# Kernel tuning notes

Measured on AMD Instinct MI355X. Metric: run time of the kernel, lower is better.

## Reference

```python
import jax, jax.numpy as jnp
import numpy as np
from jax import lax

H, E = 32, 10
ZS, ZC = 8, 8
XS, XC = 5, 2
AS, AC = 1, 4
T, N = 256, 2048


def setup_inputs() -> dict:
    key = jax.random.key(0)
    ks = jax.random.split(key, 16)
    s = 0.1
    inp = {
        'x': jax.random.uniform(ks[0], (T, N, XS, XC), jnp.float32),
        'a': jax.random.uniform(ks[1], (T, N, AS, AC), jnp.float32),
        'h0': jax.random.normal(ks[2], (N, H), jnp.float32),
        # gumbel noise for categorical sampling (argmax trick)
        'gumbel': -jnp.log(-jnp.log(jax.random.uniform(ks[3], (T, N, ZS, ZC), jnp.float32, 1e-6, 1.0 - 1e-6))),
        # Encoder: Linear(H+E -> ZS*ZC)
        'enc_W': jax.random.normal(ks[4], (ZS * ZC, H + E), jnp.float32) * s,
        'enc_b': jnp.zeros((ZS * ZC,), jnp.float32),
        # GRUCell(input = ZS*ZC + AS*AC, hidden = H)
        'gru_Wih': jax.random.normal(ks[5], (3 * H, ZS * ZC + AS * AC), jnp.float32) * s,
        'gru_Whh': jax.random.normal(ks[6], (3 * H, H), jnp.float32) * s,
        'gru_bih': jnp.zeros((3 * H,), jnp.float32),
        'gru_bhh': jnp.zeros((3 * H,), jnp.float32),
        # Decoder: Linear(H + ZS*ZC -> XS*XC)
        'dec_W': jax.random.normal(ks[7], (XS * XC, H + ZS * ZC), jnp.float32) * s,
        'dec_b': jnp.zeros((XS * XC,), jnp.float32),
        # DynamicsPredictor: Linear(H -> ZS*ZC)
        'dyn_W': jax.random.normal(ks[8], (ZS * ZC, H), jnp.float32) * s,
        'dyn_b': jnp.zeros((ZS * ZC,), jnp.float32),
        # RewardPredictor: Linear(H -> 1, no bias)
        'rew_W': jax.random.normal(ks[9], (1, H), jnp.float32) * s,
        # ContinuePredictor: Linear(H -> 1)
        'con_W': jax.random.normal(ks[10], (1, H), jnp.float32) * s,
        'con_b': jnp.zeros((1,), jnp.float32),
    }
    return inp


def _gru(x_in, h, Wih, Whh, bih, bhh):
    gi = x_in @ Wih.T + bih  # [N, 3H]
    gh = h @ Whh.T + bhh
    i_r, i_z, i_n = jnp.split(gi, 3, axis=-1)
    h_r, h_z, h_n = jnp.split(gh, 3, axis=-1)
    r = jax.nn.sigmoid(i_r + h_r)
    z = jax.nn.sigmoid(i_z + h_z)
    n = jnp.tanh(i_n + r * h_n)
    return (1.0 - z) * n + z * h


def _st_sample(logits, g):
    # OneHotCategorical straight-through sample via gumbel-argmax
    idx = jnp.argmax(logits + g, axis=-1)
    onehot = jax.nn.one_hot(idx, ZC, dtype=logits.dtype)
    probs = jax.nn.softmax(logits, axis=-1)
    return probs + lax.stop_gradient(onehot - probs)


def reference(x, a, h0, gumbel, enc_W, enc_b, gru_Wih, gru_Whh, gru_bih, gru_bhh,
              dec_W, dec_b, dyn_W, dyn_b, rew_W, con_W, con_b):
    e = x.reshape(T, N, XS * XC)        # embedder = flatten(-2)
    a_flat = a.reshape(T, N, AS * AC)

    def enc(h, e_t):
        return (jnp.concatenate([h, e_t], axis=-1) @ enc_W.T + enc_b).reshape(-1, ZS, ZC)

    zl0 = enc(h0, e[0])
    z0 = _st_sample(zl0, gumbel[0])

    def step(carry, inp):
        h_prev, z_prev = carry
        e_t, a_prev, g_t = inp
        za = jnp.concatenate([z_prev.reshape(N, ZS * ZC), a_prev], axis=-1)
        h_t = _gru(za, h_prev, gru_Wih, gru_Whh, gru_bih, gru_bhh)
        zl_t = enc(h_t, e_t)
        z_t = _st_sample(zl_t, g_t)
        return (h_t, z_t), (h_t, zl_t, z_t)

    _, (hs, zls, zs) = lax.scan(step, (h0, z0), (e[1:], a_flat[:-1], gumbel[1:]))
    h = jnp.concatenate([h0[None], hs], axis=0)                  # [T,N,H]
    z_prior_logits = jnp.concatenate([zl0[None], zls], axis=0)   # [T,N,ZS,ZC]
    z = jnp.concatenate([z0[None], zs], axis=0)                  # [T,N,ZS,ZC]

    hz = jnp.concatenate([h, z.reshape(T, N, ZS * ZC)], axis=-1)
    x_logits = (hz @ dec_W.T + dec_b).reshape(T, N, XS, XC)
    z_post_logits = (h @ dyn_W.T + dyn_b).reshape(T, N, ZS, ZC)
    r_loc = h @ rew_W.T                 # Normal loc, scale=1
    c_logits = h @ con_W.T + con_b      # Bernoulli logits
    return (x_logits, r_loc, c_logits, z_prior_logits, z_post_logits)
```

## Files before the change

kernel.cpp:

```cpp
#include <hip/hip_runtime.h>


#define TT 256
#define NB 2048
#define HH 32
#define ZD 64
#define XDm 10
#define ADm 4
#define GIN 68
#define EIN 42

#define SWHH_S 36
#define SWIH_S 97
#define SENC_S 44
#define SDYN_S 36
#define SDEC_S 100
#define SH_S   36
#define SZ_S   68

#define OFF_X   0ul
#define OFF_R   5242880ul
#define OFF_C   5767168ul
#define OFF_ZPL 6291456ul
#define OFF_ZPO 39845888ul

__device__ __forceinline__ float sigmoid_f(float v) { return 1.f / (1.f + __expf(-v)); }
__device__ __forceinline__ void nt_store(float* p, float v) { __builtin_nontemporal_store(v, p); }

extern "C" __global__ void __launch_bounds__(256)
rssm_fused(const float* __restrict__ x, const float* __restrict__ a,
           const float* __restrict__ h0, const float* __restrict__ gum,
           const float* __restrict__ encW, const float* __restrict__ encB,
           const float* __restrict__ Wih, const float* __restrict__ Whh,
           const float* __restrict__ bih, const float* __restrict__ bhh,
           const float* __restrict__ decW, const float* __restrict__ decB,
           const float* __restrict__ dynW, const float* __restrict__ dynB,
           const float* __restrict__ rewW, const float* __restrict__ conW,
           const float* __restrict__ conB, float* __restrict__ out)
{
    __shared__ __align__(16) float sWhh[96 * SWHH_S];
    __shared__ float sWih[GIN * SWIH_S];
    __shared__ __align__(16) float sEnc[64 * SENC_S];
    __shared__ __align__(16) float sDyn[64 * SDYN_S];
    __shared__ __align__(16) float sDec[10 * SDEC_S];
    __shared__ float sBih[96], sBhh[96], sEncB[64], sDynB[64], sDecB[16];
    __shared__ float sRew[32], sCon[32], sConB;
    __shared__ __align__(16) float sH[8 * SH_S];
    __shared__ float sVal[8 * 9];
    __shared__ int   sIdx[8 * 9];
    __shared__ float sZL[8 * SZ_S];
    __shared__ float sZP[8 * SZ_S];

    const int tid = threadIdx.x;

    for (int i = tid; i < 96 * HH; i += 256) { int j = i >> 5, k = i & 31; sWhh[j * SWHH_S + k] = Whh[i]; }
    for (int i = tid; i < 96 * GIN; i += 256) { int j = i / GIN, c = i - j * GIN; sWih[c * SWIH_S + j] = Wih[i]; }
    for (int i = tid; i < 64 * EIN; i += 256) { int j = i / EIN, c = i - j * EIN; sEnc[j * SENC_S + c] = encW[i]; }
    for (int i = tid; i < 64 * HH; i += 256) { int j = i >> 5, k = i & 31; sDyn[j * SDYN_S + k] = dynW[i]; }
    for (int i = tid; i < 10 * 96; i += 256) { int j = i / 96, c = i - j * 96; sDec[j * SDEC_S + c] = decW[i]; }
    if (tid < 96) { sBih[tid] = bih[tid]; sBhh[tid] = bhh[tid]; }
    if (tid >= 96 && tid < 160) { sEncB[tid - 96] = encB[tid - 96]; sDynB[tid - 96] = dynB[tid - 96]; }
    if (tid >= 160 && tid < 170) sDecB[tid - 160] = decB[tid - 160];
    if (tid >= 192 && tid < 224) sRew[tid - 192] = rewW[tid - 192];
    if (tid >= 224) sCon[tid - 224] = conW[tid - 224];
    if (tid == 170) sConB = conB[0];

    const int e    = tid & 7;
    const int slot = tid >> 3;
    const int w    = slot >> 3;
    const int r    = slot & 7;
    const int n0   = blockIdx.x * 8;
    const int n    = n0 + e;

    { int ee = tid >> 5, k = tid & 31; sH[ee * SH_S + k] = h0[(n0 + ee) * HH + k]; }
    __syncthreads();

    float h[HH];
#pragma unroll
    for (int k = 0; k < HH; k += 4) {
        float4 v = *(const float4*)&sH[e * SH_S + k];
        h[k] = v.x; h[k + 1] = v.y; h[k + 2] = v.z; h[k + 3] = v.w;
    }
    float h_own = sH[e * SH_S + slot];

    const float* xptr = x   + (size_t)n * XDm;
    const float* gptr = gum + (size_t)n * ZD;
    const float* aptr = a   + (size_t)n * ADm;

    float et[XDm], ap[ADm];
    float g1, g2;
#pragma unroll
    for (int m = 0; m < XDm; ++m) et[m] = xptr[m];
    g1 = gptr[8 * w + r];
    g2 = gptr[32 + 8 * w + r];
#pragma unroll
    for (int m = 0; m < ADm; ++m) ap[m] = 0.f;

#pragma unroll 1
    for (int t = 0; t < TT; ++t) {
        float etn[XDm], apn[ADm], g1n = 0.f, g2n = 0.f;
        if (t + 1 < TT) {
            const float* xp = xptr + (size_t)(t + 1) * (NB * XDm);
#pragma unroll
            for (int m = 0; m < XDm; ++m) etn[m] = xp[m];
            const float* gp = gptr + (size_t)(t + 1) * (NB * ZD);
            g1n = gp[8 * w + r];
            g2n = gp[32 + 8 * w + r];
            const float* app = aptr + (size_t)t * (NB * ADm);
#pragma unroll
            for (int m = 0; m < ADm; ++m) apn[m] = app[m];
        } else {
#pragma unroll
            for (int m = 0; m < XDm; ++m) etn[m] = 0.f;
#pragma unroll
            for (int m = 0; m < ADm; ++m) apn[m] = 0.f;
        }

        if (t > 0) {
            float vhr = 0.f, vhz = 0.f, vhn = 0.f;
            const float4* wr = (const float4*)&sWhh[slot * SWHH_S];
            const float4* wz = (const float4*)&sWhh[(32 + slot) * SWHH_S];
            const float4* wn = (const float4*)&sWhh[(64 + slot) * SWHH_S];
#pragma unroll
            for (int kk = 0; kk < 8; ++kk) {
                float4 wa = wr[kk], wb = wz[kk], wc = wn[kk];
                vhr = fmaf(wa.x, h[4 * kk], vhr); vhr = fmaf(wa.y, h[4 * kk + 1], vhr);
                vhr = fmaf(wa.z, h[4 * kk + 2], vhr); vhr = fmaf(wa.w, h[4 * kk + 3], vhr);
                vhz = fmaf(wb.x, h[4 * kk], vhz); vhz = fmaf(wb.y, h[4 * kk + 1], vhz);
                vhz = fmaf(wb.z, h[4 * kk + 2], vhz); vhz = fmaf(wb.w, h[4 * kk + 3], vhz);
                vhn = fmaf(wc.x, h[4 * kk], vhn); vhn = fmaf(wc.y, h[4 * kk + 1], vhn);
                vhn = fmaf(wc.z, h[4 * kk + 2], vhn); vhn = fmaf(wc.w, h[4 * kk + 3], vhn);
            }
            float vir = 0.f, viz = 0.f, vin = 0.f;
#pragma unroll
            for (int s = 0; s < 8; ++s) {
                int   c = 8 * s + sIdx[e * 9 + s];
                float v = sVal[e * 9 + s];
                const float* wc = &sWih[c * SWIH_S];
                vir = fmaf(wc[slot], v, vir);
                viz = fmaf(wc[32 + slot], v, viz);
                vin = fmaf(wc[64 + slot], v, vin);
            }
#pragma unroll
            for (int m = 0; m < ADm; ++m) {
                const float* wc = &sWih[(64 + m) * SWIH_S];
                float av = ap[m];
                vir = fmaf(wc[slot], av, vir);
                viz = fmaf(wc[32 + slot], av, viz);
                vin = fmaf(wc[64 + slot], av, vin);
            }
            float gir = vir + sBih[slot],      ghr = vhr + sBhh[slot];
            float giz = viz + sBih[32 + slot], ghz = vhz + sBhh[32 + slot];
            float gnn = vin + sBih[64 + slot], ghn = vhn + sBhh[64 + slot];
            float rg = sigmoid_f(gir + ghr);
            float zg = sigmoid_f(giz + ghz);
            float ng = tanhf(gnn + rg * ghn);
            float hn_ = (1.f - zg) * ng + zg * h_own;
            sH[e * SH_S + slot] = hn_;
        }
        __syncthreads();
        if (t > 0) {
#pragma unroll
            for (int k = 0; k < HH; k += 4) {
                float4 v = *(const float4*)&sH[e * SH_S + k];
                h[k] = v.x; h[k + 1] = v.y; h[k + 2] = v.z; h[k + 3] = v.w;
            }
            h_own = sH[e * SH_S + slot];
        }

        float z1 = 0.f, z2 = 0.f;
        {
            const float4* e1 = (const float4*)&sEnc[slot * SENC_S];
            const float4* e2 = (const float4*)&sEnc[(32 + slot) * SENC_S];
#pragma unroll
            for (int kk = 0; kk < 8; ++kk) {
                float4 wa = e1[kk], wb = e2[kk];
                z1 = fmaf(wa.x, h[4 * kk], z1); z1 = fmaf(wa.y, h[4 * kk + 1], z1);
                z1 = fmaf(wa.z, h[4 * kk + 2], z1); z1 = fmaf(wa.w, h[4 * kk + 3], z1);
                z2 = fmaf(wb.x, h[4 * kk], z2); z2 = fmaf(wb.y, h[4 * kk + 1], z2);
                z2 = fmaf(wb.z, h[4 * kk + 2], z2); z2 = fmaf(wb.w, h[4 * kk + 3], z2);
            }
            const float* e1s = &sEnc[slot * SENC_S + 32];
            const float* e2s = &sEnc[(32 + slot) * SENC_S + 32];
#pragma unroll
            for (int m = 0; m < XDm; ++m) {
                z1 = fmaf(e1s[m], et[m], z1);
                z2 = fmaf(e2s[m], et[m], z2);
            }
            z1 += sEncB[slot];
            z2 += sEncB[32 + slot];
        }

        float mx1 = z1, mx2 = z2;
#pragma unroll
        for (int d = 8; d < 64; d <<= 1) {
            mx1 = fmaxf(mx1, __shfl_xor(mx1, d));
            mx2 = fmaxf(mx2, __shfl_xor(mx2, d));
        }
        float key1 = z1 + g1; int ki1 = r;
        float key2 = z2 + g2; int ki2 = r;
#pragma unroll
        for (int d = 8; d < 64; d <<= 1) {
            float ok = __shfl_xor(key1, d); int oi = __shfl_xor(ki1, d);
            if (ok > key1 || (ok == key1 && oi < ki1)) { key1 = ok; ki1 = oi; }
            float ok2 = __shfl_xor(key2, d); int oi2 = __shfl_xor(ki2, d);
            if (ok2 > key2 || (ok2 == key2 && oi2 < ki2)) { key2 = ok2; ki2 = oi2; }
        }
        float p1 = __expf(z1 - mx1), p2 = __expf(z2 - mx2);
        float s1 = p1, s2 = p2;
#pragma unroll
        for (int d = 8; d < 64; d <<= 1) {
            s1 += __shfl_xor(s1, d);
            s2 += __shfl_xor(s2, d);
        }
        float pk1 = __shfl(p1, e + 8 * ki1) / s1;
        float pk2 = __shfl(p2, e + 8 * ki2) / s2;
        if (r == 0) {
            sVal[e * 9 + w]     = pk1 + (1.f - pk1); sIdx[e * 9 + w]     = ki1;
            sVal[e * 9 + 4 + w] = pk2 + (1.f - pk2); sIdx[e * 9 + 4 + w] = ki2;
        }
        sZL[e * SZ_S + slot]      = z1;
        sZL[e * SZ_S + 32 + slot] = z2;

        {
            float d1 = 0.f, d2 = 0.f;
            const float4* q1 = (const float4*)&sDyn[slot * SDYN_S];
            const float4* q2 = (const float4*)&sDyn[(32 + slot) * SDYN_S];
#pragma unroll
            for (int kk = 0; kk < 8; ++kk) {
                float4 wa = q1[kk], wb = q2[kk];
                d1 = fmaf(wa.x, h[4 * kk], d1); d1 = fmaf(wa.y, h[4 * kk + 1], d1);
                d1 = fmaf(wa.z, h[4 * kk + 2], d1); d1 = fmaf(wa.w, h[4 * kk + 3], d1);
                d2 = fmaf(wb.x, h[4 * kk], d2); d2 = fmaf(wb.y, h[4 * kk + 1], d2);
                d2 = fmaf(wb.z, h[4 * kk + 2], d2); d2 = fmaf(wb.w, h[4 * kk + 3], d2);
            }
            sZP[e * SZ_S + slot]      = d1 + sDynB[slot];
            sZP[e * SZ_S + 32 + slot] = d2 + sDynB[32 + slot];
        }

        __syncthreads();

        if (slot < 10) {
            const float* dw = &sDec[slot * SDEC_S];
            float acc = 0.f;
#pragma unroll
            for (int k = 0; k < HH; ++k) acc = fmaf(dw[k], h[k], acc);
#pragma unroll
            for (int s = 0; s < 8; ++s)
                acc = fmaf(dw[32 + 8 * s + sIdx[e * 9 + s]], sVal[e * 9 + s], acc);
            acc += sDecB[slot];
            nt_store(&out[OFF_X + ((size_t)t * NB + n) * XDm + slot], acc);
        } else if (slot == 10) {
            float acc = 0.f;
#pragma unroll
            for (int k = 0; k < HH; ++k) acc = fmaf(sRew[k], h[k], acc);
            nt_store(&out[OFF_R + (size_t)t * NB + n], acc);
        } else if (slot == 11) {
            float acc = 0.f;
#pragma unroll
            for (int k = 0; k < HH; ++k) acc = fmaf(sCon[k], h[k], acc);
            nt_store(&out[OFF_C + (size_t)t * NB + n], acc + sConB);
        }

        {
            size_t rowbase = (size_t)t * NB + n0;
            int f1 = tid, f2 = tid + 256;
            int ee1 = f1 >> 6, c1 = f1 & 63, ee2 = f2 >> 6, c2 = f2 & 63;
            nt_store(&out[OFF_ZPL + (rowbase + ee1) * ZD + c1], sZL[ee1 * SZ_S + c1]);
            nt_store(&out[OFF_ZPL + (rowbase + ee2) * ZD + c2], sZL[ee2 * SZ_S + c2]);
            nt_store(&out[OFF_ZPO + (rowbase + ee1) * ZD + c1], sZP[ee1 * SZ_S + c1]);
            nt_store(&out[OFF_ZPO + (rowbase + ee2) * ZD + c2], sZP[ee2 * SZ_S + c2]);
        }

#pragma unroll
        for (int m = 0; m < XDm; ++m) et[m] = etn[m];
#pragma unroll
        for (int m = 0; m < ADm; ++m) ap[m] = apn[m];
        g1 = g1n; g2 = g2n;
    }
}

extern "C" void kernel_launch(void* const* d_in, const int* in_sizes, int n_in,
                              void* d_out, int out_size, void* d_ws, size_t ws_size,
                              hipStream_t stream) {
    const float* x    = (const float*)d_in[0];
    const float* a    = (const float*)d_in[1];
    const float* h0   = (const float*)d_in[2];
    const float* gumb = (const float*)d_in[3];
    const float* encW = (const float*)d_in[4];
    const float* encB = (const float*)d_in[5];
    const float* Wih  = (const float*)d_in[6];
    const float* Whh  = (const float*)d_in[7];
    const float* bih  = (const float*)d_in[8];
    const float* bhh  = (const float*)d_in[9];
    const float* decW = (const float*)d_in[10];
    const float* decB = (const float*)d_in[11];
    const float* dynW = (const float*)d_in[12];
    const float* dynB = (const float*)d_in[13];
    const float* rewW = (const float*)d_in[14];
    const float* conW = (const float*)d_in[15];
    const float* conB = (const float*)d_in[16];

    rssm_fused<<<NB / 8, 256, 0, stream>>>(x, a, h0, gumb, encW, encB, Wih, Whh,
                                           bih, bhh, decW, decB, dynW, dynB,
                                           rewW, conW, conB, (float*)d_out);
}
```

Baseline: 1.191 ms.

## Map one batch element per wavefront to remove block-wide barriers

Restructures the recurrent kernel so that each 64-lane wavefront owns one batch element, where before 8 elements were spread across the whole 256-thread block. The per-step block barriers and the shared buffers for logits and samples are replaced by wave shuffles and register copies. Each lane now computes one encoder and one dynamics output, and the output stores are issued directly and coalesced. The grid doubles and the launch bounds request two blocks per CU. The cost is that each lane runs longer serial dot products: it handles two of the three GRU gates, using a shuffle for the z gate, with scalar strided shared-memory reads.

```diff
diff --git a/kernel.cpp b/kernel.cpp
--- a/kernel.cpp
+++ b/kernel.cpp
@@ -7,16 +7,13 @@
 #define ZD 64
 #define XDm 10
 #define ADm 4
-#define GIN 68
-#define EIN 42
-
-#define SWHH_S 36
+
+#define SWHH_S 37
 #define SWIH_S 97
-#define SENC_S 44
-#define SDYN_S 36
-#define SDEC_S 100
-#define SH_S   36
-#define SZ_S   68
+#define SENC_S 45
+#define SDYN_S 37
+#define SDEC_S 97
+#define SH_S   40
 
 #define OFF_X   0ul
 #define OFF_R   5242880ul
@@ -27,7 +24,7 @@
 __device__ __forceinline__ float sigmoid_f(float v) { return 1.f / (1.f + __expf(-v)); }
 __device__ __forceinline__ void nt_store(float* p, float v) { __builtin_nontemporal_store(v, p); }
 
-extern "C" __global__ void __launch_bounds__(256)
+extern "C" __global__ void __launch_bounds__(256, 2)
 rssm_fused(const float* __restrict__ x, const float* __restrict__ a,
            const float* __restrict__ h0, const float* __restrict__ gum,
            const float* __restrict__ encW, const float* __restrict__ encB,
@@ -38,24 +35,20 @@
            const float* __restrict__ rewW, const float* __restrict__ conW,
            const float* __restrict__ conB, float* __restrict__ out)
 {
-    __shared__ __align__(16) float sWhh[96 * SWHH_S];
-    __shared__ float sWih[GIN * SWIH_S];
-    __shared__ __align__(16) float sEnc[64 * SENC_S];
-    __shared__ __align__(16) float sDyn[64 * SDYN_S];
-    __shared__ __align__(16) float sDec[10 * SDEC_S];
+    __shared__ float sWhh[96 * SWHH_S];
+    __shared__ float sWih[68 * SWIH_S];
+    __shared__ float sEnc[64 * SENC_S];
+    __shared__ float sDyn[64 * SDYN_S];
+    __shared__ float sDec[10 * SDEC_S];
     __shared__ float sBih[96], sBhh[96], sEncB[64], sDynB[64], sDecB[16];
     __shared__ float sRew[32], sCon[32], sConB;
-    __shared__ __align__(16) float sH[8 * SH_S];
-    __shared__ float sVal[8 * 9];
-    __shared__ int   sIdx[8 * 9];
-    __shared__ float sZL[8 * SZ_S];
-    __shared__ float sZP[8 * SZ_S];
+    __shared__ __align__(16) float sH[4 * SH_S];
 
     const int tid = threadIdx.x;
 
     for (int i = tid; i < 96 * HH; i += 256) { int j = i >> 5, k = i & 31; sWhh[j * SWHH_S + k] = Whh[i]; }
-    for (int i = tid; i < 96 * GIN; i += 256) { int j = i / GIN, c = i - j * GIN; sWih[c * SWIH_S + j] = Wih[i]; }
-    for (int i = tid; i < 64 * EIN; i += 256) { int j = i / EIN, c = i - j * EIN; sEnc[j * SENC_S + c] = encW[i]; }
+    for (int i = tid; i < 96 * 68; i += 256) { int j = i / 68, c = i - j * 68; sWih[c * SWIH_S + j] = Wih[i]; }
+    for (int i = tid; i < 64 * 42; i += 256) { int j = i / 42, c = i - j * 42; sEnc[j * SENC_S + c] = encW[i]; }
     for (int i = tid; i < 64 * HH; i += 256) { int j = i >> 5, k = i & 31; sDyn[j * SDYN_S + k] = dynW[i]; }
     for (int i = tid; i < 10 * 96; i += 256) { int j = i / 96, c = i - j * 96; sDec[j * SDEC_S + c] = decW[i]; }
     if (tid < 96) { sBih[tid] = bih[tid]; sBhh[tid] = bhh[tid]; }
@@ -65,48 +58,49 @@
     if (tid >= 224) sCon[tid - 224] = conW[tid - 224];
     if (tid == 170) sConB = conB[0];
 
-    const int e    = tid & 7;
-    const int slot = tid >> 3;
-    const int w    = slot >> 3;
-    const int r    = slot & 7;
-    const int n0   = blockIdx.x * 8;
-    const int n    = n0 + e;
-
-    { int ee = tid >> 5, k = tid & 31; sH[ee * SH_S + k] = h0[(n0 + ee) * HH + k]; }
+    const int wv  = tid >> 6;
+    const int l   = tid & 63;
+    const int j32 = l & 31;
+    const int grp = l >> 3;
+    const int gl  = l & 7;
+    const int n   = blockIdx.x * 4 + wv;
+
     __syncthreads();
 
-    float h[HH];
-#pragma unroll
-    for (int k = 0; k < HH; k += 4) {
-        float4 v = *(const float4*)&sH[e * SH_S + k];
-        h[k] = v.x; h[k + 1] = v.y; h[k + 2] = v.z; h[k + 3] = v.w;
+    float h[HH], h_own;
+    {
+        float h0v = 0.f;
+        if (l < HH) { h0v = h0[(size_t)n * HH + l]; sH[wv * SH_S + l] = h0v; }
+#pragma unroll
+        for (int k = 0; k < HH; k += 4) {
+            float4 v = *(const float4*)&sH[wv * SH_S + k];
+            h[k] = v.x; h[k + 1] = v.y; h[k + 2] = v.z; h[k + 3] = v.w;
+        }
+        h_own = h0v;
     }
-    float h_own = sH[e * SH_S + slot];
-
-    const float* xptr = x   + (size_t)n * XDm;
-    const float* gptr = gum + (size_t)n * ZD;
-    const float* aptr = a   + (size_t)n * ADm;
-
-    float et[XDm], ap[ADm];
-    float g1, g2;
-#pragma unroll
-    for (int m = 0; m < XDm; ++m) et[m] = xptr[m];
-    g1 = gptr[8 * w + r];
-    g2 = gptr[32 + 8 * w + r];
+
+    const float* xb = x + (size_t)n * XDm;
+    const float* ab = a + (size_t)n * ADm;
+
+    float et[XDm], ap[ADm], gv;
+    float sv[8]; int si[8];
+#pragma unroll
+    for (int s = 0; s < 8; ++s) { sv[s] = 0.f; si[s] = 0; }
+#pragma unroll
+    for (int m = 0; m < XDm; ++m) et[m] = xb[m];
+    gv = gum[(size_t)n * ZD + l];
 #pragma unroll
     for (int m = 0; m < ADm; ++m) ap[m] = 0.f;
 
 #pragma unroll 1
     for (int t = 0; t < TT; ++t) {
-        float etn[XDm], apn[ADm], g1n = 0.f, g2n = 0.f;
+        float etn[XDm], apn[ADm], gvn = 0.f;
         if (t + 1 < TT) {
-            const float* xp = xptr + (size_t)(t + 1) * (NB * XDm);
+            const float* xp = xb + (size_t)(t + 1) * (NB * XDm);
 #pragma unroll
             for (int m = 0; m < XDm; ++m) etn[m] = xp[m];
-            const float* gp = gptr + (size_t)(t + 1) * (NB * ZD);
-            g1n = gp[8 * w + r];
-            g2n = gp[32 + 8 * w + r];
-            const float* app = aptr + (size_t)t * (NB * ADm);
+            gvn = gum[((size_t)(t + 1) * NB + n) * ZD + l];
+            const float* app = ab + (size_t)t * (NB * ADm);
 #pragma unroll
             for (int m = 0; m < ADm; ++m) apn[m] = app[m];
         } else {
@@ -117,166 +111,111 @@
         }
 
         if (t > 0) {
-            float vhr = 0.f, vhz = 0.f, vhn = 0.f;
-            const float4* wr = (const float4*)&sWhh[slot * SWHH_S];
-            const float4* wz = (const float4*)&sWhh[(32 + slot) * SWHH_S];
-            const float4* wn = (const float4*)&sWhh[(64 + slot) * SWHH_S];
-#pragma unroll
-            for (int kk = 0; kk < 8; ++kk) {
-                float4 wa = wr[kk], wb = wz[kk], wc = wn[kk];
-                vhr = fmaf(wa.x, h[4 * kk], vhr); vhr = fmaf(wa.y, h[4 * kk + 1], vhr);
-                vhr = fmaf(wa.z, h[4 * kk + 2], vhr); vhr = fmaf(wa.w, h[4 * kk + 3], vhr);
-                vhz = fmaf(wb.x, h[4 * kk], vhz); vhz = fmaf(wb.y, h[4 * kk + 1], vhz);
-                vhz = fmaf(wb.z, h[4 * kk + 2], vhz); vhz = fmaf(wb.w, h[4 * kk + 3], vhz);
-                vhn = fmaf(wc.x, h[4 * kk], vhn); vhn = fmaf(wc.y, h[4 * kk + 1], vhn);
-                vhn = fmaf(wc.z, h[4 * kk + 2], vhn); vhn = fmaf(wc.w, h[4 * kk + 3], vhn);
-            }
-            float vir = 0.f, viz = 0.f, vin = 0.f;
+            const float* wA = &sWhh[l * SWHH_S];
+            const float* wB = &sWhh[(64 + j32) * SWHH_S];
+            float accA = 0.f, accB = 0.f;
+#pragma unroll
+            for (int k = 0; k < HH; ++k) {
+                accA = fmaf(wA[k], h[k], accA);
+                accB = fmaf(wB[k], h[k], accB);
+            }
+            float giA = 0.f, giB = 0.f;
 #pragma unroll
             for (int s = 0; s < 8; ++s) {
-                int   c = 8 * s + sIdx[e * 9 + s];
-                float v = sVal[e * 9 + s];
+                int   c = 8 * s + si[s];
+                float v = sv[s];
                 const float* wc = &sWih[c * SWIH_S];
-                vir = fmaf(wc[slot], v, vir);
-                viz = fmaf(wc[32 + slot], v, viz);
-                vin = fmaf(wc[64 + slot], v, vin);
+                giA = fmaf(wc[l], v, giA);
+                giB = fmaf(wc[64 + j32], v, giB);
             }
 #pragma unroll
             for (int m = 0; m < ADm; ++m) {
                 const float* wc = &sWih[(64 + m) * SWIH_S];
-                float av = ap[m];
-                vir = fmaf(wc[slot], av, vir);
-                viz = fmaf(wc[32 + slot], av, viz);
-                vin = fmaf(wc[64 + slot], av, vin);
-            }
-            float gir = vir + sBih[slot],      ghr = vhr + sBhh[slot];
-            float giz = viz + sBih[32 + slot], ghz = vhz + sBhh[32 + slot];
-            float gnn = vin + sBih[64 + slot], ghn = vhn + sBhh[64 + slot];
-            float rg = sigmoid_f(gir + ghr);
-            float zg = sigmoid_f(giz + ghz);
-            float ng = tanhf(gnn + rg * ghn);
-            float hn_ = (1.f - zg) * ng + zg * h_own;
-            sH[e * SH_S + slot] = hn_;
-        }
-        __syncthreads();
-        if (t > 0) {
+                giA = fmaf(wc[l], ap[m], giA);
+                giB = fmaf(wc[64 + j32], ap[m], giB);
+            }
+            giA += sBih[l];        float ghA = accA + sBhh[l];
+            giB += sBih[64 + j32]; float ghB = accB + sBhh[64 + j32];
+            float sA = sigmoid_f(giA + ghA);
+            float zj = __shfl(sA, l | 32);
+            float ng = tanhf(giB + sA * ghB);
+            float hn = (1.f - zj) * ng + zj * h_own;
+            if (l < HH) sH[wv * SH_S + l] = hn;
 #pragma unroll
             for (int k = 0; k < HH; k += 4) {
-                float4 v = *(const float4*)&sH[e * SH_S + k];
+                float4 v = *(const float4*)&sH[wv * SH_S + k];
                 h[k] = v.x; h[k + 1] = v.y; h[k + 2] = v.z; h[k + 3] = v.w;
             }
-            h_own = sH[e * SH_S + slot];
-        }
-
-        float z1 = 0.f, z2 = 0.f;
+            h_own = hn;
+        }
+
+        float z;
         {
-            const float4* e1 = (const float4*)&sEnc[slot * SENC_S];
-            const float4* e2 = (const float4*)&sEnc[(32 + slot) * SENC_S];
-#pragma unroll
-            for (int kk = 0; kk < 8; ++kk) {
-                float4 wa = e1[kk], wb = e2[kk];
-                z1 = fmaf(wa.x, h[4 * kk], z1); z1 = fmaf(wa.y, h[4 * kk + 1], z1);
-                z1 = fmaf(wa.z, h[4 * kk + 2], z1); z1 = fmaf(wa.w, h[4 * kk + 3], z1);
-                z2 = fmaf(wb.x, h[4 * kk], z2); z2 = fmaf(wb.y, h[4 * kk + 1], z2);
-                z2 = fmaf(wb.z, h[4 * kk + 2], z2); z2 = fmaf(wb.w, h[4 * kk + 3], z2);
-            }
-            const float* e1s = &sEnc[slot * SENC_S + 32];
-            const float* e2s = &sEnc[(32 + slot) * SENC_S + 32];
-#pragma unroll
-            for (int m = 0; m < XDm; ++m) {
-                z1 = fmaf(e1s[m], et[m], z1);
-                z2 = fmaf(e2s[m], et[m], z2);
-            }
-            z1 += sEncB[slot];
-            z2 += sEncB[32 + slot];
-        }
-
-        float mx1 = z1, mx2 = z2;
-#pragma unroll
-        for (int d = 8; d < 64; d <<= 1) {
-            mx1 = fmaxf(mx1, __shfl_xor(mx1, d));
-            mx2 = fmaxf(mx2, __shfl_xor(mx2, d));
-        }
-        float key1 = z1 + g1; int ki1 = r;
-        float key2 = z2 + g2; int ki2 = r;
-#pragma unroll
-        for (int d = 8; d < 64; d <<= 1) {
-            float ok = __shfl_xor(key1, d); int oi = __shfl_xor(ki1, d);
-            if (ok > key1 || (ok == key1 && oi < ki1)) { key1 = ok; ki1 = oi; }
-            float ok2 = __shfl_xor(key2, d); int oi2 = __shfl_xor(ki2, d);
-            if (ok2 > key2 || (ok2 == key2 && oi2 < ki2)) { key2 = ok2; ki2 = oi2; }
-        }
-        float p1 = __expf(z1 - mx1), p2 = __expf(z2 - mx2);
-        float s1 = p1, s2 = p2;
-#pragma unroll
-        for (int d = 8; d < 64; d <<= 1) {
-            s1 += __shfl_xor(s1, d);
-            s2 += __shfl_xor(s2, d);
-        }
-        float pk1 = __shfl(p1, e + 8 * ki1) / s1;
-        float pk2 = __shfl(p2, e + 8 * ki2) / s2;
-        if (r == 0) {
-            sVal[e * 9 + w]     = pk1 + (1.f - pk1); sIdx[e * 9 + w]     = ki1;
-            sVal[e * 9 + 4 + w] = pk2 + (1.f - pk2); sIdx[e * 9 + 4 + w] = ki2;
-        }
-        sZL[e * SZ_S + slot]      = z1;
-        sZL[e * SZ_S + 32 + slot] = z2;
+            const float* we = &sEnc[l * SENC_S];
+            float acc = 0.f;
+#pragma unroll
+            for (int k = 0; k < HH; ++k) acc = fmaf(we[k], h[k], acc);
+#pragma unroll
+            for (int m = 0; m < XDm; ++m) acc = fmaf(we[HH + m], et[m], acc);
+            z = acc + sEncB[l];
+        }
+
+        float mx = z;
+#pragma unroll
+        for (int d = 1; d < 8; d <<= 1) mx = fmaxf(mx, __shfl_xor(mx, d));
+        float key = z + gv; int ki = gl;
+#pragma unroll
+        for (int d = 1; d < 8; d <<= 1) {
+            float ok = __shfl_xor(key, d); int oi = __shfl_xor(ki, d);
+            if (ok > key || (ok == key && oi < ki)) { key = ok; ki = oi; }
+        }
+        float p = __expf(z - mx);
+        float ssum = p;
+#pragma unroll
+        for (int d = 1; d < 8; d <<= 1) ssum += __shfl_xor(ssum, d);
+        float pk  = __shfl(p, (grp << 3) + ki) / ssum;
+        float val = pk + (1.f - pk);
+#pragma unroll
+        for (int s = 0; s < 8; ++s) {
+            sv[s] = __shfl(val, s << 3);
+            si[s] = __shfl(ki,  s << 3);
+        }
+
+        nt_store(&out[OFF_ZPL + ((size_t)t * NB + n) * ZD + l], z);
 
         {
-            float d1 = 0.f, d2 = 0.f;
-            const float4* q1 = (const float4*)&sDyn[slot * SDYN_S];
-            const float4* q2 = (const float4*)&sDyn[(32 + slot) * SDYN_S];
-#pragma unroll
-            for (int kk = 0; kk < 8; ++kk) {
-                float4 wa = q1[kk], wb = q2[kk];
-                d1 = fmaf(wa.x, h[4 * kk], d1); d1 = fmaf(wa.y, h[4 * kk + 1], d1);
-                d1 = fmaf(wa.z, h[4 * kk + 2], d1); d1 = fmaf(wa.w, h[4 * kk + 3], d1);
-                d2 = fmaf(wb.x, h[4 * kk], d2); d2 = fmaf(wb.y, h[4 * kk + 1], d2);
-                d2 = fmaf(wb.z, h[4 * kk + 2], d2); d2 = fmaf(wb.w, h[4 * kk + 3], d2);
-            }
-            sZP[e * SZ_S + slot]      = d1 + sDynB[slot];
-            sZP[e * SZ_S + 32 + slot] = d2 + sDynB[32 + slot];
-        }
-
-        __syncthreads();
-
-        if (slot < 10) {
-            const float* dw = &sDec[slot * SDEC_S];
+            const float* wd = &sDyn[l * SDYN_S];
+            float acc = 0.f;
+#pragma unroll
+            for (int k = 0; k < HH; ++k) acc = fmaf(wd[k], h[k], acc);
+            nt_store(&out[OFF_ZPO + ((size_t)t * NB + n) * ZD + l], acc + sDynB[l]);
+        }
+
+        if (l < XDm) {
+            const float* dw = &sDec[l * SDEC_S];
             float acc = 0.f;
 #pragma unroll
             for (int k = 0; k < HH; ++k) acc = fmaf(dw[k], h[k], acc);
 #pragma unroll
             for (int s = 0; s < 8; ++s)
-                acc = fmaf(dw[32 + 8 * s + sIdx[e * 9 + s]], sVal[e * 9 + s], acc);
-            acc += sDecB[slot];
-            nt_store(&out[OFF_X + ((size_t)t * NB + n) * XDm + slot], acc);
-        } else if (slot == 10) {
-            float acc = 0.f;
-#pragma unroll
-            for (int k = 0; k < HH; ++k) acc = fmaf(sRew[k], h[k], acc);
-            nt_store(&out[OFF_R + (size_t)t * NB + n], acc);
-        } else if (slot == 11) {
-            float acc = 0.f;
-#pragma unroll
-            for (int k = 0; k < HH; ++k) acc = fmaf(sCon[k], h[k], acc);
-            nt_store(&out[OFF_C + (size_t)t * NB + n], acc + sConB);
-        }
-
-        {
-            size_t rowbase = (size_t)t * NB + n0;
-            int f1 = tid, f2 = tid + 256;
-            int ee1 = f1 >> 6, c1 = f1 & 63, ee2 = f2 >> 6, c2 = f2 & 63;
-            nt_store(&out[OFF_ZPL + (rowbase + ee1) * ZD + c1], sZL[ee1 * SZ_S + c1]);
-            nt_store(&out[OFF_ZPL + (rowbase + ee2) * ZD + c2], sZL[ee2 * SZ_S + c2]);
-            nt_store(&out[OFF_ZPO + (rowbase + ee1) * ZD + c1], sZP[ee1 * SZ_S + c1]);
-            nt_store(&out[OFF_ZPO + (rowbase + ee2) * ZD + c2], sZP[ee2 * SZ_S + c2]);
+                acc = fmaf(dw[HH + 8 * s + si[s]], sv[s], acc);
+            acc += sDecB[l];
+            nt_store(&out[OFF_X + ((size_t)t * NB + n) * XDm + l], acc);
+        } else if (l >= 10 && l < 12) {
+            const float* hw = (l == 10) ? sRew : sCon;
+            float acc = 0.f;
+#pragma unroll
+            for (int k = 0; k < HH; ++k) acc = fmaf(hw[k], h[k], acc);
+            if (l == 11) acc += sConB;
+            size_t off = (l == 10) ? OFF_R : OFF_C;
+            nt_store(&out[off + (size_t)t * NB + n], acc);
         }
 
 #pragma unroll
         for (int m = 0; m < XDm; ++m) et[m] = etn[m];
 #pragma unroll
         for (int m = 0; m < ADm; ++m) ap[m] = apn[m];
-        g1 = g1n; g2 = g2n;
+        gv = gvn;
     }
 }
 
@@ -301,7 +240,7 @@
     const float* conW = (const float*)d_in[15];
     const float* conB = (const float*)d_in[16];
 
-    rssm_fused<<<NB / 8, 256, 0, stream>>>(x, a, h0, gumb, encW, encB, Wih, Whh,
+    rssm_fused<<<NB / 4, 256, 0, stream>>>(x, a, h0, gumb, encW, encB, Wih, Whh,
                                            bih, bhh, decW, decB, dynW, dynB,
                                            rewW, conW, conB, (float*)d_out);
 }
```

New measurement: 1.014 ms. -14.8%, faster.
